# Performance work log

Hardware: AMD Instinct MI355X
Metric: run time of the kernel (lower is better)

Reference implementation:

```python
import jax, jax.numpy as jnp
import numpy as np

N = 100000
IN_CH = 128
OUT_CH = 32
HEADS = 4
E = 1600000
NEG_SLOPE = 0.2  # PyG GATConv default negative_slope


def setup_inputs() -> dict:
    key = jax.random.key(0)
    k_x, k_e, k_w, k_as, k_ad, k_b = jax.random.split(key, 6)
    x = jax.random.normal(k_x, (N, IN_CH), dtype=jnp.float32)
    edge_index = jax.random.randint(k_e, (2, E), 0, N, dtype=jnp.int64)
    # Glorot-style scale for linear weight, small normals for attention vectors
    W = jax.random.normal(k_w, (IN_CH, HEADS * OUT_CH), dtype=jnp.float32) * (1.0 / np.sqrt(IN_CH))
    att_src = jax.random.normal(k_as, (1, HEADS, OUT_CH), dtype=jnp.float32) * 0.1
    att_dst = jax.random.normal(k_ad, (1, HEADS, OUT_CH), dtype=jnp.float32) * 0.1
    bias = jnp.zeros((HEADS * OUT_CH,), dtype=jnp.float32)
    return {"x": x, "edge_index": edge_index, "W": W,
            "att_src": att_src, "att_dst": att_dst, "bias": bias}


def reference(x, edge_index, W, att_src, att_dst, bias):
    n = x.shape[0]
    # Linear transform: [N, H, C]
    xw = (x @ W).reshape(n, HEADS, OUT_CH)
    # Per-node attention logits: [N, H]
    a_src = (xw * att_src).sum(-1)
    a_dst = (xw * att_dst).sum(-1)
    # Add self-loops (PyG GATConv default add_self_loops=True)
    loop = jnp.arange(n, dtype=edge_index.dtype)
    src = jnp.concatenate([edge_index[0], loop])  # [E']
    dst = jnp.concatenate([edge_index[1], loop])  # [E']
    # Edge-wise attention logits + leaky relu: [E', H]
    alpha = jax.nn.leaky_relu(a_src[src] + a_dst[dst], NEG_SLOPE)
    # Segment softmax over edges grouped by destination node
    amax = jax.ops.segment_max(alpha, dst, num_segments=n)
    alpha = jnp.exp(alpha - amax[dst])
    denom = jax.ops.segment_sum(alpha, dst, num_segments=n)
    alpha = alpha / (denom[dst] + 1e-16)
    # Weighted scatter-aggregate of source features: [N, H, C]
    msg = xw[src] * alpha[:, :, None]
    out = jax.ops.segment_sum(msg, dst, num_segments=n)
    out = out.reshape(n, HEADS * OUT_CH) + bias
    return jax.nn.elu(out)
```

## Files before the change

### kernel.cpp

```cpp
#include <hip/hip_runtime.h>
#include <cmath>


#define LOG2E 1.44269504088896340736f

typedef float f32x2 __attribute__((ext_vector_type(2)));
typedef float f32x4 __attribute__((ext_vector_type(4)));

__device__ __forceinline__ float fast_exp2(float x) {
#if __has_builtin(__builtin_amdgcn_exp2f)
  return __builtin_amdgcn_exp2f(x);
#else
  return exp2f(x);
#endif
}

__device__ __forceinline__ unsigned bf16_rne(float f) {
  unsigned u = __float_as_uint(f);
  return (u + 0x7fffu + ((u >> 16) & 1u)) >> 16;
}
__device__ __forceinline__ float bf_lo(unsigned v) {
  return __uint_as_float(v << 16);
}
__device__ __forceinline__ float bf_hi(unsigned v) {
  return __uint_as_float(v & 0xffff0000u);
}

__device__ __forceinline__ int blockInclScan(int v, int tid, int* lds) {
  int lane = tid & 63;
  int wid = tid >> 6;
#pragma unroll
  for (int off = 1; off < 64; off <<= 1) {
    int t = __shfl_up(v, off);
    if (lane >= off) v += t;
  }
  if (lane == 63) lds[wid] = v;
  __syncthreads();
  int add = 0;
  for (int i = 0; i < wid; ++i) add += lds[i];
  v += add;
  __syncthreads();
  return v;
}

#define CHUNK 4096
#define MAXE 3072

__global__ __launch_bounds__(256) void k_hist(const int* __restrict__ ei, int E,
                                              int EL, int NB, int NBLK,
                                              int* __restrict__ bh,
                                              int* __restrict__ btot) {
  __shared__ int lh[512];
  int tid = threadIdx.x;
  lh[tid] = 0;
  lh[tid + 256] = 0;
  __syncthreads();
  int base_e = blockIdx.x * CHUNK;
#pragma unroll
  for (int j = 0; j < CHUNK / 256; ++j) {
    int e = base_e + j * 256 + tid;
    if (e < EL) {
      int dst = (e < E) ? ei[E + e] : (e - E);
      atomicAdd(&lh[dst >> 8], 1);
    }
  }
  __syncthreads();
  for (int b = tid; b < NB; b += 256) {
    int c = lh[b];
    bh[(size_t)b * NBLK + blockIdx.x] = c;
    if (c) atomicAdd(&btot[b], c);
  }
}

__global__ __launch_bounds__(256) void p2c_brow(int* __restrict__ bh,
                                                const int* __restrict__ btot,
                                                int* __restrict__ bbase,
                                                int NB, int NBLK) {
  __shared__ int lds[4];
  __shared__ int ctot;
  __shared__ int red[256];
  int b = blockIdx.x;
  int tid = threadIdx.x;
  int part = 0;
  for (int j = tid; j < b; j += 256) part += btot[j];
  red[tid] = part;
  __syncthreads();
  for (int st = 128; st > 0; st >>= 1) {
    if (tid < st) red[tid] += red[tid + st];
    __syncthreads();
  }
  int base = red[0];
  if (tid == 0) bbase[b] = base;
  __syncthreads();
  int v0 = (tid < NBLK) ? bh[(size_t)b * NBLK + tid] : 0;
  int incl0 = blockInclScan(v0, tid, lds);
  if (tid < NBLK) bh[(size_t)b * NBLK + tid] = base + incl0 - v0;
  if (tid == 255) ctot = incl0;
  __syncthreads();
  int base1 = base + ctot;
  int j = 256 + tid;
  int v1 = (j < NBLK) ? bh[(size_t)b * NBLK + j] : 0;
  int incl1 = blockInclScan(v1, tid, lds);
  if (j < NBLK) bh[(size_t)b * NBLK + j] = base1 + incl1 - v1;
}

__global__ __launch_bounds__(256) void k_fusedB(
    const float* __restrict__ x, const float* __restrict__ Wm,
    const float* __restrict__ att_src, const float* __restrict__ att_dst,
    unsigned* __restrict__ xwb, float* __restrict__ a_src,
    float* __restrict__ a_dst, int N, int GB,
    const int* __restrict__ ei, int E, int EL, int NB, int NBLK,
    const int* __restrict__ bh, unsigned* __restrict__ tmp) {
  __shared__ __align__(16) char sm[33280];
  const int tid = threadIdx.x;

  if ((int)blockIdx.x >= GB) {
    int blk = blockIdx.x - GB;
    int* lc = (int*)sm;
    for (int b = tid; b < NB; b += 256) lc[b] = bh[(size_t)b * NBLK + blk];
    __syncthreads();
    int base_e = blk * CHUNK;
#pragma unroll
    for (int j = 0; j < CHUNK / 256; ++j) {
      int e = base_e + j * 256 + tid;
      if (e < EL) {
        int src, dst;
        if (e < E) {
          src = ei[e];
          dst = ei[E + e];
        } else {
          src = e - E;
          dst = e - E;
        }
        int pos = atomicAdd(&lc[dst >> 8], 1);
        tmp[pos] = ((unsigned)(dst & 255) << 24) | (unsigned)src;
      }
    }
    return;
  }

  float (*xs_t)[132] = (float(*)[132])sm;
  float (*Wl)[128] = (float(*)[128])(sm + 16896);
  const int tx = tid & 15;
  const int ty = tid >> 4;
  const int row0 = blockIdx.x * 128;

  float acc[8][8];
#pragma unroll
  for (int r = 0; r < 8; ++r)
#pragma unroll
    for (int c = 0; c < 8; ++c) acc[r][c] = 0.f;

  for (int kc = 0; kc < 4; ++kc) {
    __syncthreads();
#pragma unroll
    for (int j = 0; j < 4; ++j) {
      int f = tid + j * 256;
      int r = f >> 3, k4 = f & 7;
      int row = row0 + r;
      float4 v = make_float4(0.f, 0.f, 0.f, 0.f);
      if (row < N) v = *(const float4*)&x[(size_t)row * 128 + kc * 32 + k4 * 4];
      xs_t[k4 * 4 + 0][r] = v.x;
      xs_t[k4 * 4 + 1][r] = v.y;
      xs_t[k4 * 4 + 2][r] = v.z;
      xs_t[k4 * 4 + 3][r] = v.w;
    }
#pragma unroll
    for (int j = 0; j < 4; ++j) {
      int f = tid + j * 256;
      int kr = f >> 5, c4 = f & 31;
      *(float4*)&Wl[kr][c4 * 4] =
          *(const float4*)&Wm[(size_t)(kc * 32 + kr) * 128 + c4 * 4];
    }
    __syncthreads();
#pragma unroll 4
    for (int k = 0; k < 32; ++k) {
      float wv[8], xv[8];
      *(float4*)&wv[0] = *(const float4*)&Wl[k][tx * 8];
      *(float4*)&wv[4] = *(const float4*)&Wl[k][tx * 8 + 4];
      *(float4*)&xv[0] = *(const float4*)&xs_t[k][ty * 8];
      *(float4*)&xv[4] = *(const float4*)&xs_t[k][ty * 8 + 4];
#pragma unroll
      for (int r = 0; r < 8; ++r)
#pragma unroll
        for (int c = 0; c < 8; ++c) acc[r][c] = fmaf(xv[r], wv[c], acc[r][c]);
    }
  }

  float att_s[8], att_d[8];
#pragma unroll
  for (int c = 0; c < 8; ++c) {
    att_s[c] = att_src[tx * 8 + c];
    att_d[c] = att_dst[tx * 8 + c];
  }

#pragma unroll
  for (int r = 0; r < 8; ++r) {
    int row = row0 + ty * 8 + r;
    bool ok = row < N;
    float vs = 0.f, vd = 0.f;
#pragma unroll
    for (int c = 0; c < 8; ++c) {
      vs += acc[r][c] * att_s[c];
      vd += acc[r][c] * att_d[c];
    }
    vs += __shfl_xor(vs, 1);
    vs += __shfl_xor(vs, 2);
    vd += __shfl_xor(vd, 1);
    vd += __shfl_xor(vd, 2);
    if (ok) {
      uint4 pk;
      pk.x = bf16_rne(acc[r][0]) | (bf16_rne(acc[r][1]) << 16);
      pk.y = bf16_rne(acc[r][2]) | (bf16_rne(acc[r][3]) << 16);
      pk.z = bf16_rne(acc[r][4]) | (bf16_rne(acc[r][5]) << 16);
      pk.w = bf16_rne(acc[r][6]) | (bf16_rne(acc[r][7]) << 16);
      *(uint4*)&xwb[(size_t)row * 64 + tx * 4] = pk;
      if ((tx & 3) == 0) {
        a_src[row * 4 + (tx >> 2)] = vs * LOG2E;
        a_dst[row * 4 + (tx >> 2)] = vd * LOG2E;
      }
    }
  }
}

__global__ __launch_bounds__(256) void k_bagg(
    const unsigned* __restrict__ tmp, const int* __restrict__ bbase,
    const int* __restrict__ btot, const float* __restrict__ asrc,
    const float* __restrict__ adst, const unsigned* __restrict__ xwb,
    const float* __restrict__ bias, float* __restrict__ out, int N) {
  __shared__ unsigned sorted[MAXE];
  __shared__ int deg[64];
  __shared__ int startd[64];
  __shared__ int cur[64];
  const int bid = blockIdx.x;
  const int b = bid >> 2;
  const int p = bid & 3;
  const int tid = threadIdx.x;
  const int beg = bbase[b];
  const int cnt = btot[b];
  if (tid < 64) deg[tid] = 0;
  __syncthreads();
  for (int k = tid; k < cnt; k += 256) {
    unsigned w = tmp[beg + k];
    int dloc = w >> 24;
    if ((dloc >> 6) == p) atomicAdd(&deg[dloc & 63], 1);
  }
  __syncthreads();
  if (tid < 64) {
    int v = deg[tid];
    int incl = v;
#pragma unroll
    for (int off = 1; off < 64; off <<= 1) {
      int t = __shfl_up(incl, off);
      if (tid >= off) incl += t;
    }
    int excl = incl - v;
    startd[tid] = excl;
    cur[tid] = excl;
  }
  __syncthreads();
  for (int k = tid; k < cnt; k += 256) {
    unsigned w = tmp[beg + k];
    int dloc = w >> 24;
    if ((dloc >> 6) == p) {
      int pos = atomicAdd(&cur[dloc & 63], 1);
      if (pos < MAXE) sorted[pos] = w;
    }
  }
  __syncthreads();
  const int wv = tid >> 6;
  const int lane = tid & 63;
  const int half = lane >> 5;
  const int l5 = lane & 31;
  const int h = l5 >> 3;
  const unsigned* xr = xwb + l5 * 2;
  const float4 bv = *(const float4*)&bias[l5 * 4];

  for (int j = 0; j < 16; ++j) {
    int dl = wv + 4 * j;
    int gdst = b * 256 + p * 64 + dl;
    if (gdst >= N) break;
    int sd = startd[dl];
    int ed = min(sd + deg[dl], MAXE);
    float ad = adst[gdst * 4 + h];

    float sA = 0.f, sB = 0.f;
    float a0 = 0.f, a1 = 0.f, a2 = 0.f, a3 = 0.f;
    float b0 = 0.f, b1 = 0.f, b2 = 0.f, b3 = 0.f;
    int i = sd + half;
    for (; i + 6 < ed; i += 8) {
      unsigned wA = sorted[i], wB = sorted[i + 2];
      unsigned wC = sorted[i + 4], wD = sorted[i + 6];
      int eA = wA & 0xFFFFFF, eB = wB & 0xFFFFFF;
      int eC = wC & 0xFFFFFF, eD = wD & 0xFFFFFF;
      float tA = asrc[eA * 4 + h] + ad;
      float tB = asrc[eB * 4 + h] + ad;
      float tC = asrc[eC * 4 + h] + ad;
      float tD = asrc[eD * 4 + h] + ad;
      uint2 vA = *(const uint2*)(xr + (size_t)eA * 64);
      uint2 vB = *(const uint2*)(xr + (size_t)eB * 64);
      uint2 vC = *(const uint2*)(xr + (size_t)eC * 64);
      uint2 vD = *(const uint2*)(xr + (size_t)eD * 64);
      float pA = fast_exp2(fmaxf(tA, 0.2f * tA));
      float pB = fast_exp2(fmaxf(tB, 0.2f * tB));
      float pC = fast_exp2(fmaxf(tC, 0.2f * tC));
      float pD = fast_exp2(fmaxf(tD, 0.2f * tD));
      sA += pA + pC;
      sB += pB + pD;
      a0 = fmaf(pA, bf_lo(vA.x), a0);
      a1 = fmaf(pA, bf_hi(vA.x), a1);
      a2 = fmaf(pA, bf_lo(vA.y), a2);
      a3 = fmaf(pA, bf_hi(vA.y), a3);
      b0 = fmaf(pB, bf_lo(vB.x), b0);
      b1 = fmaf(pB, bf_hi(vB.x), b1);
      b2 = fmaf(pB, bf_lo(vB.y), b2);
      b3 = fmaf(pB, bf_hi(vB.y), b3);
      a0 = fmaf(pC, bf_lo(vC.x), a0);
      a1 = fmaf(pC, bf_hi(vC.x), a1);
      a2 = fmaf(pC, bf_lo(vC.y), a2);
      a3 = fmaf(pC, bf_hi(vC.y), a3);
      b0 = fmaf(pD, bf_lo(vD.x), b0);
      b1 = fmaf(pD, bf_hi(vD.x), b1);
      b2 = fmaf(pD, bf_lo(vD.y), b2);
      b3 = fmaf(pD, bf_hi(vD.y), b3);
    }
    for (; i < ed; i += 2) {
      unsigned wA = sorted[i];
      int eA = wA & 0xFFFFFF;
      float tA = asrc[eA * 4 + h] + ad;
      uint2 vA = *(const uint2*)(xr + (size_t)eA * 64);
      float pA = fast_exp2(fmaxf(tA, 0.2f * tA));
      sA += pA;
      a0 = fmaf(pA, bf_lo(vA.x), a0);
      a1 = fmaf(pA, bf_hi(vA.x), a1);
      a2 = fmaf(pA, bf_lo(vA.y), a2);
      a3 = fmaf(pA, bf_hi(vA.y), a3);
    }
    float s = sA + sB;
    a0 += b0;
    a1 += b1;
    a2 += b2;
    a3 += b3;
    s += __shfl_xor(s, 32);
    a0 += __shfl_xor(a0, 32);
    a1 += __shfl_xor(a1, 32);
    a2 += __shfl_xor(a2, 32);
    a3 += __shfl_xor(a3, 32);

    if (half == 0) {
      float inv = 1.f / s;
      float o0 = fmaf(a0, inv, bv.x);
      float o1 = fmaf(a1, inv, bv.y);
      float o2 = fmaf(a2, inv, bv.z);
      float o3 = fmaf(a3, inv, bv.w);
      o0 = o0 > 0.f ? o0 : fast_exp2(o0 * LOG2E) - 1.f;
      o1 = o1 > 0.f ? o1 : fast_exp2(o1 * LOG2E) - 1.f;
      o2 = o2 > 0.f ? o2 : fast_exp2(o2 * LOG2E) - 1.f;
      o3 = o3 > 0.f ? o3 : fast_exp2(o3 * LOG2E) - 1.f;
      f32x4 o = {o0, o1, o2, o3};
      __builtin_nontemporal_store(o, (f32x4*)&out[(size_t)gdst * 128 + l5 * 4]);
    }
  }
}

extern "C" void kernel_launch(void* const* d_in, const int* in_sizes, int n_in,
                              void* d_out, int out_size, void* d_ws, size_t ws_size,
                              hipStream_t stream) {
  const float* x = (const float*)d_in[0];
  const int* ei = (const int*)d_in[1];
  const float* Wm = (const float*)d_in[2];
  const float* att_src = (const float*)d_in[3];
  const float* att_dst = (const float*)d_in[4];
  const float* bias = (const float*)d_in[5];
  float* out = (float*)d_out;

  const int N = in_sizes[0] / 128;
  const int E = in_sizes[1] / 2;
  const int EL = E + N;
  const int NB = (N + 255) >> 8;
  const int NBLK = (EL + CHUNK - 1) / CHUNK;
  const int GB = (N + 127) / 128;

  size_t off = 0;
  auto carve = [&](size_t bytes) -> void* {
    void* p = (char*)d_ws + off;
    off += (bytes + 255) & ~(size_t)255;
    return p;
  };
  unsigned* xwb = (unsigned*)carve((size_t)N * 64 * 4);
  float* a_src = (float*)carve((size_t)N * 4 * 4);
  float* a_dst = (float*)carve((size_t)N * 4 * 4);
  unsigned* tmp = (unsigned*)carve((size_t)EL * 4);
  int* bh = (int*)carve((size_t)NB * NBLK * 4);
  int* btot = (int*)carve((size_t)NB * 4);
  int* bbase = (int*)carve((size_t)NB * 4);

  (void)hipMemsetAsync(btot, 0, (size_t)NB * 4, stream);

  k_hist<<<NBLK, 256, 0, stream>>>(ei, E, EL, NB, NBLK, bh, btot);
  p2c_brow<<<NB, 256, 0, stream>>>(bh, btot, bbase, NB, NBLK);
  k_fusedB<<<GB + NBLK, 256, 0, stream>>>(x, Wm, att_src, att_dst, xwb, a_src,
                                          a_dst, N, GB, ei, E, EL, NB, NBLK,
                                          bh, tmp);
  k_bagg<<<NB * 4, 256, 0, stream>>>(tmp, bbase, btot, a_src, a_dst, xwb,
                                     bias, out, N);
}
```

Measured before the change: 174.1 us.

## Bucket edges by 64-node groups to drop redundant bucket scans in aggregation

Destination buckets shrink from 256 nodes to 64, so each aggregation block owns exactly one bucket. Before, four blocks each scanned the full 256-node bucket's edge list twice and discarded three quarters of it. Each edge word now packs a 6-bit local destination and a 17-bit source index. In exchange the histogram has four times as many bins, which enlarges the per-chunk offset table and the prefix-scan work. The 17-bit source field also limits N to 131072.

After: 178.8 us. +2.7%, slower.

```diff
diff --git a/kernel.cpp b/kernel.cpp
--- a/kernel.cpp
+++ b/kernel.cpp
@@ -44,16 +44,15 @@
 }
 
 #define CHUNK 4096
-#define MAXE 3072
+#define MAXE 2560
 
 __global__ __launch_bounds__(256) void k_hist(const int* __restrict__ ei, int E,
-                                              int EL, int NB, int NBLK,
+                                              int EL, int NB2, int NBLK,
                                               int* __restrict__ bh,
                                               int* __restrict__ btot) {
-  __shared__ int lh[512];
+  __shared__ int lh[1792];
   int tid = threadIdx.x;
-  lh[tid] = 0;
-  lh[tid + 256] = 0;
+  for (int b = tid; b < NB2; b += 256) lh[b] = 0;
   __syncthreads();
   int base_e = blockIdx.x * CHUNK;
 #pragma unroll
@@ -61,11 +60,11 @@
     int e = base_e + j * 256 + tid;
     if (e < EL) {
       int dst = (e < E) ? ei[E + e] : (e - E);
-      atomicAdd(&lh[dst >> 8], 1);
-    }
-  }
-  __syncthreads();
-  for (int b = tid; b < NB; b += 256) {
+      atomicAdd(&lh[dst >> 6], 1);
+    }
+  }
+  __syncthreads();
+  for (int b = tid; b < NB2; b += 256) {
     int c = lh[b];
     bh[(size_t)b * NBLK + blockIdx.x] = c;
     if (c) atomicAdd(&btot[b], c);
@@ -75,7 +74,7 @@
 __global__ __launch_bounds__(256) void p2c_brow(int* __restrict__ bh,
                                                 const int* __restrict__ btot,
                                                 int* __restrict__ bbase,
-                                                int NB, int NBLK) {
+                                                int NB2, int NBLK) {
   __shared__ int lds[4];
   __shared__ int ctot;
   __shared__ int red[256];
@@ -109,7 +108,7 @@
     const float* __restrict__ att_src, const float* __restrict__ att_dst,
     unsigned* __restrict__ xwb, float* __restrict__ a_src,
     float* __restrict__ a_dst, int N, int GB,
-    const int* __restrict__ ei, int E, int EL, int NB, int NBLK,
+    const int* __restrict__ ei, int E, int EL, int NB2, int NBLK,
     const int* __restrict__ bh, unsigned* __restrict__ tmp) {
   __shared__ __align__(16) char sm[33280];
   const int tid = threadIdx.x;
@@ -117,7 +116,7 @@
   if ((int)blockIdx.x >= GB) {
     int blk = blockIdx.x - GB;
     int* lc = (int*)sm;
-    for (int b = tid; b < NB; b += 256) lc[b] = bh[(size_t)b * NBLK + blk];
+    for (int b = tid; b < NB2; b += 256) lc[b] = bh[(size_t)b * NBLK + blk];
     __syncthreads();
     int base_e = blk * CHUNK;
 #pragma unroll
@@ -132,8 +131,8 @@
           src = e - E;
           dst = e - E;
         }
-        int pos = atomicAdd(&lc[dst >> 8], 1);
-        tmp[pos] = ((unsigned)(dst & 255) << 24) | (unsigned)src;
+        int pos = atomicAdd(&lc[dst >> 6], 1);
+        tmp[pos] = ((unsigned)(dst & 63) << 17) | (unsigned)src;
       }
     }
     return;
@@ -233,17 +232,14 @@
   __shared__ int startd[64];
   __shared__ int cur[64];
   const int bid = blockIdx.x;
-  const int b = bid >> 2;
-  const int p = bid & 3;
   const int tid = threadIdx.x;
-  const int beg = bbase[b];
-  const int cnt = btot[b];
+  const int beg = bbase[bid];
+  const int cnt = btot[bid];
   if (tid < 64) deg[tid] = 0;
   __syncthreads();
   for (int k = tid; k < cnt; k += 256) {
     unsigned w = tmp[beg + k];
-    int dloc = w >> 24;
-    if ((dloc >> 6) == p) atomicAdd(&deg[dloc & 63], 1);
+    atomicAdd(&deg[w >> 17], 1);
   }
   __syncthreads();
   if (tid < 64) {
@@ -261,11 +257,8 @@
   __syncthreads();
   for (int k = tid; k < cnt; k += 256) {
     unsigned w = tmp[beg + k];
-    int dloc = w >> 24;
-    if ((dloc >> 6) == p) {
-      int pos = atomicAdd(&cur[dloc & 63], 1);
-      if (pos < MAXE) sorted[pos] = w;
-    }
+    int pos = atomicAdd(&cur[w >> 17], 1);
+    if (pos < MAXE) sorted[pos] = w;
   }
   __syncthreads();
   const int wv = tid >> 6;
@@ -278,7 +271,7 @@
 
   for (int j = 0; j < 16; ++j) {
     int dl = wv + 4 * j;
-    int gdst = b * 256 + p * 64 + dl;
+    int gdst = bid * 64 + dl;
     if (gdst >= N) break;
     int sd = startd[dl];
     int ed = min(sd + deg[dl], MAXE);
@@ -291,8 +284,8 @@
     for (; i + 6 < ed; i += 8) {
       unsigned wA = sorted[i], wB = sorted[i + 2];
       unsigned wC = sorted[i + 4], wD = sorted[i + 6];
-      int eA = wA & 0xFFFFFF, eB = wB & 0xFFFFFF;
-      int eC = wC & 0xFFFFFF, eD = wD & 0xFFFFFF;
+      int eA = wA & 0x1FFFF, eB = wB & 0x1FFFF;
+      int eC = wC & 0x1FFFF, eD = wD & 0x1FFFF;
       float tA = asrc[eA * 4 + h] + ad;
       float tB = asrc[eB * 4 + h] + ad;
       float tC = asrc[eC * 4 + h] + ad;
@@ -326,7 +319,7 @@
     }
     for (; i < ed; i += 2) {
       unsigned wA = sorted[i];
-      int eA = wA & 0xFFFFFF;
+      int eA = wA & 0x1FFFF;
       float tA = asrc[eA * 4 + h] + ad;
       uint2 vA = *(const uint2*)(xr + (size_t)eA * 64);
       float pA = fast_exp2(fmaxf(tA, 0.2f * tA));
@@ -377,7 +370,7 @@
   const int N = in_sizes[0] / 128;
   const int E = in_sizes[1] / 2;
   const int EL = E + N;
-  const int NB = (N + 255) >> 8;
+  const int NB2 = (N + 63) >> 6;
   const int NBLK = (EL + CHUNK - 1) / CHUNK;
   const int GB = (N + 127) / 128;
 
@@ -391,17 +384,17 @@
   float* a_src = (float*)carve((size_t)N * 4 * 4);
   float* a_dst = (float*)carve((size_t)N * 4 * 4);
   unsigned* tmp = (unsigned*)carve((size_t)EL * 4);
-  int* bh = (int*)carve((size_t)NB * NBLK * 4);
-  int* btot = (int*)carve((size_t)NB * 4);
-  int* bbase = (int*)carve((size_t)NB * 4);
-
-  (void)hipMemsetAsync(btot, 0, (size_t)NB * 4, stream);
-
-  k_hist<<<NBLK, 256, 0, stream>>>(ei, E, EL, NB, NBLK, bh, btot);
-  p2c_brow<<<NB, 256, 0, stream>>>(bh, btot, bbase, NB, NBLK);
+  int* bh = (int*)carve((size_t)NB2 * NBLK * 4);
+  int* btot = (int*)carve((size_t)NB2 * 4);
+  int* bbase = (int*)carve((size_t)NB2 * 4);
+
+  (void)hipMemsetAsync(btot, 0, (size_t)NB2 * 4, stream);
+
+  k_hist<<<NBLK, 256, 0, stream>>>(ei, E, EL, NB2, NBLK, bh, btot);
+  p2c_brow<<<NB2, 256, 0, stream>>>(bh, btot, bbase, NB2, NBLK);
   k_fusedB<<<GB + NBLK, 256, 0, stream>>>(x, Wm, att_src, att_dst, xwb, a_src,
-                                          a_dst, N, GB, ei, E, EL, NB, NBLK,
+                                          a_dst, N, GB, ei, E, EL, NB2, NBLK,
                                           bh, tmp);
-  k_bagg<<<NB * 4, 256, 0, stream>>>(tmp, bbase, btot, a_src, a_dst, xwb,
-                                     bias, out, N);
-}
+  k_bagg<<<NB2, 256, 0, stream>>>(tmp, bbase, btot, a_src, a_dst, xwb,
+                                  bias, out, N);
+}
```
